# Kernel tuning notes

Measured on AMD Instinct MI355X. Metric: run time of the kernel, lower is better.

## Reference

```python
import jax, jax.numpy as jnp
import numpy as np

B, T, DK, DV, N = 4, 1024, 128, 128, 65536
TOPK = 32

def setup_inputs() -> dict:
    key = jax.random.key(0)
    k1, k2, k3 = jax.random.split(key, 3)
    q = jax.random.normal(k1, (B, T, DK), dtype=jnp.float32)
    keys = jax.random.normal(k2, (N, DK), dtype=jnp.float32)
    values = jax.random.normal(k3, (N, DV), dtype=jnp.float32)
    return {"q": q, "keys": keys, "values": values, "topk": TOPK}

def reference(q, keys, values, topk):
    # scores: [B, T, N] dense dot-product score matrix
    scores = jnp.einsum('btd,nd->btn', q, keys)
    k = min(topk, keys.shape[0])
    _, idx = jax.lax.top_k(scores, k)          # idx: [B, T, k]
    K_mem = keys[idx]                          # [B, T, k, Dk] gather
    V_mem = values[idx]                        # [B, T, k, Dv] gather
    return (K_mem, V_mem)
```

## Files before the change

### kernel.cpp

```cpp
#include <hip/hip_runtime.h>
#include <float.h>

#define NQ      4096
#define NKEYS   65536
#define DKDIM   128
#define DVDIM   128
#define TOPK_N  32
#define NSPLIT  16
#define KPS     (NKEYS / NSPLIT)
#define BQ      128
#define NCAND   (NSPLIT * TOPK_N)
#define NARROW  64
#define NOUT    ((size_t)NQ * TOPK_N * DKDIM)
#define KPT     64
#define NT      (KPS / KPT)

typedef __attribute__((ext_vector_type(8))) short short8;
typedef __attribute__((ext_vector_type(4))) float v4f;

__device__ inline unsigned short f2bf(float f) {
    unsigned int u = __float_as_uint(f);
    return (unsigned short)((u + 0x7FFFu + ((u >> 16) & 1u)) >> 16);
}

__device__ inline unsigned packpk(float s, unsigned li) {
    unsigned u = __float_as_uint(s);
    u = ((int)u < 0) ? ~u : (u | 0x80000000u);
    return (u & 0xFFFFF000u) | (4095u - li);
}
__device__ inline float unpack_lb(unsigned pk) {
    const unsigned m = pk & 0xFFFFF000u;
    const unsigned b = (m & 0x80000000u) ? (m & 0x7FFFFFFFu) : ~m;
    return __uint_as_float(b);
}

#define CEXU(p, s, desc) {                                                  \
    const unsigned _o = (unsigned)__shfl_xor((int)(p), (s));                \
    const bool _first = (p) > _o;                                           \
    const bool _keep  = (_first == (((l16 & (s)) == 0) == (desc)));         \
    (p) = _keep ? (p) : _o; }
#define CEXUI(pa, pb) { if ((pb) > (pa)) { const unsigned _t=(pa); (pa)=(pb); (pb)=_t; } }

__device__ __forceinline__ void sortmergeU(
    unsigned& p0, unsigned& p1, const int cc,
    const unsigned* __restrict__ bqr, const int l16)
{
    unsigned s0 = (l16      < cc) ? bqr[l16]      : 0u;
    unsigned s1 = (l16 + 16 < cc) ? bqr[l16 + 16] : 0u;

    CEXU(s0, 1, ((l16 & 2) == 0)); CEXU(s1, 1, ((l16 & 2) == 0));
    CEXU(s0, 2, ((l16 & 4) == 0)); CEXU(s1, 2, ((l16 & 4) == 0));
    CEXU(s0, 1, ((l16 & 4) == 0)); CEXU(s1, 1, ((l16 & 4) == 0));
    CEXU(s0, 4, ((l16 & 8) == 0)); CEXU(s1, 4, ((l16 & 8) == 0));
    CEXU(s0, 2, ((l16 & 8) == 0)); CEXU(s1, 2, ((l16 & 8) == 0));
    CEXU(s0, 1, ((l16 & 8) == 0)); CEXU(s1, 1, ((l16 & 8) == 0));
    CEXU(s0, 8, true);  CEXU(s1, 8, false);
    CEXU(s0, 4, true);  CEXU(s1, 4, false);
    CEXU(s0, 2, true);  CEXU(s1, 2, false);
    CEXU(s0, 1, true);  CEXU(s1, 1, false);
    CEXUI(s0, s1);
    CEXU(s0, 8, true);  CEXU(s1, 8, true);
    CEXU(s0, 4, true);  CEXU(s1, 4, true);
    CEXU(s0, 2, true);  CEXU(s1, 2, true);
    CEXU(s0, 1, true);  CEXU(s1, 1, true);

    unsigned c0 = (unsigned)__shfl_xor((int)s1, 15);
    unsigned c1 = (unsigned)__shfl_xor((int)s0, 15);

    CEXUI(p0, c0);
    CEXUI(p1, c1);
    CEXUI(p0, p1);
    CEXU(p0, 8, true); CEXU(p1, 8, true);
    CEXU(p0, 4, true); CEXU(p1, 4, true);
    CEXU(p0, 2, true); CEXU(p1, 2, true);
    CEXU(p0, 1, true); CEXU(p1, 1, true);
}

__global__ __launch_bounds__(256) void convert_kernel(
    const float* __restrict__ q, const float* __restrict__ keys,
    unsigned short* __restrict__ qbf, unsigned short* __restrict__ kbf)
{
    const size_t QG = (size_t)NQ * DKDIM / 8;
    const size_t KG = (size_t)NKEYS * DKDIM / 8;
    const size_t g  = (size_t)blockIdx.x * 256 + threadIdx.x;
    if (g >= QG + KG) return;
    const float* src;
    unsigned short* dst;
    if (g < QG) { src = q + g * 8;         dst = qbf + g * 8; }
    else        { const size_t h = g - QG; src = keys + h * 8; dst = kbf + h * 8; }
    const float4 a = ((const float4*)src)[0];
    const float4 b = ((const float4*)src)[1];
    short8 o;
    o[0] = (short)f2bf(a.x); o[1] = (short)f2bf(a.y);
    o[2] = (short)f2bf(a.z); o[3] = (short)f2bf(a.w);
    o[4] = (short)f2bf(b.x); o[5] = (short)f2bf(b.y);
    o[6] = (short)f2bf(b.z); o[7] = (short)f2bf(b.w);
    *(short8*)dst = o;
}

__global__ __launch_bounds__(512, 4) void score_select_kernel(
    const unsigned short* __restrict__ qbf, const unsigned short* __restrict__ kbf,
    unsigned* __restrict__ cand)
{
    __shared__ unsigned short kst[2][KPT * DKDIM];
    __shared__ unsigned bq[BQ][33];

    const int tid  = threadIdx.x;
    const int wave = tid >> 6;
    const int lane = tid & 63;
    const int l16  = lane & 15;
    const int quad = lane >> 4;

    const int lin   = blockIdx.y * gridDim.x + blockIdx.x;
    const int split = ((lin & 7) << 1) | (lin >> 8);
    const int qgrp  = (lin >> 3) & 31;
    const int q0    = qgrp * BQ + wave * 16;
    const int nbase = split * KPS;

    unsigned* __restrict__ bqr = &bq[wave * 16 + l16][0];

    short8 afrag[4];
#pragma unroll
    for (int t = 0; t < 4; ++t)
        afrag[t] = *(const short8*)(qbf + (size_t)(q0 + l16) * DKDIM + t * 32 + quad * 8);

    unsigned pk0[4], pk1[4];
#pragma unroll
    for (int r = 0; r < 4; ++r) { pk0[r] = 0u; pk1[r] = 0u; }
    float vmf = -FLT_MAX;
    int   cnt = 0;

    auto select32 = [&](const v4f a1, const v4f a2, const int n0loc) {
        const int h0 = a1[0] > vmf, h1 = a1[1] > vmf, h2 = a1[2] > vmf, h3 = a1[3] > vmf;
        const int h4 = a2[0] > vmf, h5 = a2[1] > vmf, h6 = a2[2] > vmf, h7 = a2[3] > vmf;
        const int nh = h0 + h1 + h2 + h3 + h4 + h5 + h6 + h7;
        const int s16   = __shfl_xor(nh, 16);
        const int psum  = nh + s16;
        const int sx32  = __shfl_xor(psum, 32);
        const int nhcol = psum + sx32;
        if (__ballot(cnt + nhcol > 32)) {
#pragma unroll
            for (int r = 0; r < 4; ++r) {
                const int cc = __shfl(cnt, quad * 4 + r);
                sortmergeU(pk0[r], pk1[r], cc, &bq[wave * 16 + quad * 4 + r][0], l16);
            }
            const unsigned t0 = (unsigned)__shfl((int)pk1[0], (l16 >> 2) * 16 + 15);
            const unsigned t1 = (unsigned)__shfl((int)pk1[1], (l16 >> 2) * 16 + 15);
            const unsigned t2 = (unsigned)__shfl((int)pk1[2], (l16 >> 2) * 16 + 15);
            const unsigned t3 = (unsigned)__shfl((int)pk1[3], (l16 >> 2) * 16 + 15);
            const unsigned a01 = (l16 & 1) ? t1 : t0;
            const unsigned a23 = (l16 & 1) ? t3 : t2;
            vmf = unpack_lb((l16 & 2) ? a23 : a01);
            cnt = 0;
        }
        int pos = cnt + ((quad & 1) ? s16 : 0) + ((quad & 2) ? sx32 : 0);
        const unsigned lb = (unsigned)(n0loc + quad * 4);
        if (h0) { bqr[pos] = packpk(a1[0], lb);      ++pos; }
        if (h1) { bqr[pos] = packpk(a1[1], lb + 1);  ++pos; }
        if (h2) { bqr[pos] = packpk(a1[2], lb + 2);  ++pos; }
        if (h3) { bqr[pos] = packpk(a1[3], lb + 3);  ++pos; }
        if (h4) { bqr[pos] = packpk(a2[0], lb + 16); ++pos; }
        if (h5) { bqr[pos] = packpk(a2[1], lb + 17); ++pos; }
        if (h6) { bqr[pos] = packpk(a2[2], lb + 18); ++pos; }
        if (h7) { bqr[pos] = packpk(a2[3], lb + 19); }
        cnt += nhcol;
    };

    const unsigned short* ksrc = kbf + (size_t)nbase * DKDIM;
    const int c0 = tid, c1 = tid + 512;
    const int d0 = ((c0 >> 4) * 128) + (((c0 & 15) ^ ((c0 >> 4) & 7)) * 8);
    const int d1 = ((c1 >> 4) * 128) + (((c1 & 15) ^ ((c1 >> 4) & 7)) * 8);
    const int sx = l16 & 7;

    {
        const short8 a = *(const short8*)(ksrc + c0 * 8);
        const short8 b = *(const short8*)(ksrc + c1 * 8);
        *(short8*)&kst[0][d0] = a;
        *(short8*)&kst[0][d1] = b;
    }
    __syncthreads();

    int cur = 0;
    for (int t = 0; t < NT; ++t) {
        short8 nA, nB;
        const bool more = (t + 1 < NT);
        if (more) {
            const unsigned short* s = ksrc + (size_t)(t + 1) * (KPT * DKDIM);
            nA = *(const short8*)(s + c0 * 8);
            nB = *(const short8*)(s + c1 * 8);
        }
#pragma unroll
        for (int half = 0; half < 2; ++half) {
            const unsigned short* kr0 = &kst[cur][(half * 32 + l16) * 128];
            const unsigned short* kr1 = &kst[cur][(half * 32 + 16 + l16) * 128];
            v4f acc1 = {0.f, 0.f, 0.f, 0.f};
            v4f acc2 = {0.f, 0.f, 0.f, 0.f};
#pragma unroll
            for (int tt = 0; tt < 4; ++tt) {
                const short8 b0 = *(const short8*)(kr0 + ((quad + tt * 4) ^ sx) * 8);
                const short8 b1 = *(const short8*)(kr1 + ((quad + tt * 4) ^ sx) * 8);
                acc1 = __builtin_amdgcn_mfma_f32_16x16x32_bf16(b0, afrag[tt], acc1, 0, 0, 0);
                acc2 = __builtin_amdgcn_mfma_f32_16x16x32_bf16(b1, afrag[tt], acc2, 0, 0, 0);
            }
            select32(acc1, acc2, t * KPT + half * 32);
        }
        if (more) {
            *(short8*)&kst[cur ^ 1][d0] = nA;
            *(short8*)&kst[cur ^ 1][d1] = nB;
        }
        __syncthreads();
        cur ^= 1;
    }

#pragma unroll
    for (int r = 0; r < 4; ++r) {
        const int cc = __shfl(cnt, quad * 4 + r);
        sortmergeU(pk0[r], pk1[r], cc, &bq[wave * 16 + quad * 4 + r][0], l16);
        const size_t base = ((size_t)(q0 + quad * 4 + r) * NSPLIT + split) * TOPK_N;
        cand[base + l16]      = pk0[r];
        cand[base + 16 + l16] = pk1[r];
    }
}

__global__ __launch_bounds__(512) void rescore_gather_kernel(
    const float* __restrict__ qg, const float* __restrict__ keys,
    const float* __restrict__ values, const unsigned* __restrict__ cand,
    float* __restrict__ out)
{
    __shared__ float    qrow[DKDIM];
    __shared__ unsigned spk[NCAND];
    __shared__ int      spn[NCAND];
    __shared__ int      ssi[TOPK_N];
    const int bt  = blockIdx.x;
    const int tid = threadIdx.x;

    if (tid < DKDIM) qrow[tid] = qg[(size_t)bt * DKDIM + tid];

    unsigned pk = cand[(size_t)bt * NCAND + tid];
    int      n  = (tid >> 5) * KPS + (int)(4095u - (pk & 0xFFFu));

    for (int k = 2; k <= NCAND; k <<= 1) {
        for (int j = k >> 1; j > 0; j >>= 1) {
            unsigned opk; int on;
            if (j >= 64) {
                __syncthreads();
                spk[tid] = pk; spn[tid] = n;
                __syncthreads();
                opk = spk[tid ^ j]; on = spn[tid ^ j];
            } else {
                opk = (unsigned)__shfl_xor((int)pk, j);
                on  = __shfl_xor(n, j);
            }
            const bool dir  = ((tid & k) == 0);
            const bool mineFirst = (pk > opk) || (pk == opk && n < on);
            const bool keep = (((tid & j) == 0) == (mineFirst == dir));
            if (!keep) { pk = opk; n = on; }
        }
    }
    __syncthreads();

    float sc = -FLT_MAX;
    if (tid < NARROW) {
        const float4* krow = (const float4*)(keys + (size_t)n * DKDIM);
        float s = 0.f;
#pragma unroll
        for (int d4 = 0; d4 < DKDIM / 4; ++d4) {
            const float4 k4 = krow[d4];
            const float4 q4 = *(const float4*)&qrow[4 * d4];
            s = fmaf(q4.x, k4.x, s);
            s = fmaf(q4.y, k4.y, s);
            s = fmaf(q4.z, k4.z, s);
            s = fmaf(q4.w, k4.w, s);
        }
        sc = s;
    }

    if (tid < 64) {
        for (int k = 2; k <= NARROW; k <<= 1) {
            for (int j = k >> 1; j > 0; j >>= 1) {
                const float of = __shfl_xor(sc, j);
                const int   on = __shfl_xor(n, j);
                const bool dir  = ((tid & k) == 0);
                const bool mineFirst = (sc > of) || (sc == of && n < on);
                const bool keep = (((tid & j) == 0) == (mineFirst == dir));
                if (!keep) { sc = of; n = on; }
            }
        }
        if (tid < TOPK_N) ssi[tid] = n;
    }
    __syncthreads();

    const int lane = tid & 31;
    const int rb   = tid >> 5;
#pragma unroll
    for (int r = 0; r < 2; ++r) {
        const int row = rb + 16 * r;
        const int nn  = ssi[row];
        const float4 kv = *(const float4*)(keys   + (size_t)nn * DKDIM + 4 * lane);
        const float4 vv = *(const float4*)(values + (size_t)nn * DVDIM + 4 * lane);
        const size_t ob = ((size_t)bt * TOPK_N + row) * DKDIM + 4 * lane;
        *(float4*)(out + ob)        = kv;
        *(float4*)(out + NOUT + ob) = vv;
    }
}

extern "C" void kernel_launch(void* const* d_in, const int* in_sizes, int n_in,
                              void* d_out, int out_size, void* d_ws, size_t ws_size,
                              hipStream_t stream)
{
    const float* q      = (const float*)d_in[0];
    const float* keys   = (const float*)d_in[1];
    const float* values = (const float*)d_in[2];
    float* out = (float*)d_out;

    unsigned short* qbf = (unsigned short*)d_ws;
    unsigned short* kbf = (unsigned short*)((char*)d_ws + (1u << 20));
    unsigned* cand = (unsigned*)((char*)d_ws + (17u << 20));

    const int cvt_groups = (NQ + NKEYS) * DKDIM / 8;
    convert_kernel<<<(cvt_groups + 255) / 256, 256, 0, stream>>>(q, keys, qbf, kbf);
    score_select_kernel<<<dim3(NQ / BQ, NSPLIT), 512, 0, stream>>>(qbf, kbf, cand);
    rescore_gather_kernel<<<NQ, 512, 0, stream>>>(q, keys, values, cand, out);
}
```

Measured before the change: 534.3 us.

## Sort candidates per wave in registers, removing block-level syncs in rescore

The rescore/gather kernel now gives each query to a single 64-lane wave, with four queries per 256-thread block, instead of one query per 512-thread block. The 512-candidate bitonic sort runs with each lane holding eight elements in registers. Strides of 64 and above become in-register compare-swaps, so the shared-memory exchange and __syncthreads pairs go away. The wave keeps the top 64 by approximate score, rescores them in fp32, and sorts and gathers without any block barrier. The cost is more registers per thread and more shuffle work per wave, in exchange for fewer barriers and less shared memory.

Result: no change. 542.7 us (+1.6%).

```diff
diff --git a/kernel.cpp b/kernel.cpp
--- a/kernel.cpp
+++ b/kernel.cpp
@@ -10,7 +10,6 @@
 #define KPS     (NKEYS / NSPLIT)
 #define BQ      128
 #define NCAND   (NSPLIT * TOPK_N)
-#define NARROW  64
 #define NOUT    ((size_t)NQ * TOPK_N * DKDIM)
 #define KPT     64
 #define NT      (KPS / KPT)
@@ -222,51 +221,99 @@
     }
 }
 
-__global__ __launch_bounds__(512) void rescore_gather_kernel(
+__global__ __launch_bounds__(256) void rescore_gather_kernel(
     const float* __restrict__ qg, const float* __restrict__ keys,
     const float* __restrict__ values, const unsigned* __restrict__ cand,
     float* __restrict__ out)
 {
-    __shared__ float    qrow[DKDIM];
-    __shared__ unsigned spk[NCAND];
-    __shared__ int      spn[NCAND];
-    __shared__ int      ssi[TOPK_N];
-    const int bt  = blockIdx.x;
-    const int tid = threadIdx.x;
-
-    if (tid < DKDIM) qrow[tid] = qg[(size_t)bt * DKDIM + tid];
-
-    unsigned pk = cand[(size_t)bt * NCAND + tid];
-    int      n  = (tid >> 5) * KPS + (int)(4095u - (pk & 0xFFFu));
-
-    for (int k = 2; k <= NCAND; k <<= 1) {
+    __shared__ float qsh[4][DKDIM];
+    const int tid  = threadIdx.x;
+    const int wave = tid >> 6;
+    const int lane = tid & 63;
+    const int qidx = blockIdx.x * 4 + wave;
+
+    qsh[wave][lane]      = qg[(size_t)qidx * DKDIM + lane];
+    qsh[wave][lane + 64] = qg[(size_t)qidx * DKDIM + lane + 64];
+    __syncthreads();
+
+    unsigned pk[8]; int nn[8];
+#pragma unroll
+    for (int i = 0; i < 8; ++i) {
+        const int e = i * 64 + lane;
+        const unsigned p = cand[(size_t)qidx * NCAND + e];
+        pk[i] = p;
+        nn[i] = (e >> 5) * KPS + (int)(4095u - (p & 0xFFFu));
+    }
+
+#pragma unroll
+    for (int k = 2; k <= 256; k <<= 1) {
+#pragma unroll
         for (int j = k >> 1; j > 0; j >>= 1) {
-            unsigned opk; int on;
             if (j >= 64) {
-                __syncthreads();
-                spk[tid] = pk; spn[tid] = n;
-                __syncthreads();
-                opk = spk[tid ^ j]; on = spn[tid ^ j];
+                const int m = j >> 6;
+#pragma unroll
+                for (int i = 0; i < 8; ++i) {
+                    if ((i & m) == 0) {
+                        const int i2 = i | m;
+                        const bool dir = (((i << 6) & k) == 0);
+                        const bool first = (pk[i] > pk[i2]) ||
+                                           (pk[i] == pk[i2] && nn[i] < nn[i2]);
+                        if (first != dir) {
+                            const unsigned tp = pk[i]; pk[i] = pk[i2]; pk[i2] = tp;
+                            const int      tn = nn[i]; nn[i] = nn[i2]; nn[i2] = tn;
+                        }
+                    }
+                }
             } else {
-                opk = (unsigned)__shfl_xor((int)pk, j);
-                on  = __shfl_xor(n, j);
+#pragma unroll
+                for (int i = 0; i < 8; ++i) {
+                    const unsigned opk = (unsigned)__shfl_xor((int)pk[i], j);
+                    const int      onn = __shfl_xor(nn[i], j);
+                    const bool dir   = ((((i << 6) | lane) & k) == 0);
+                    const bool upper = ((lane & j) == 0);
+                    const bool mineFirst = (pk[i] > opk) ||
+                                           (pk[i] == opk && nn[i] < onn);
+                    if (upper != (mineFirst == dir)) { pk[i] = opk; nn[i] = onn; }
+                }
             }
-            const bool dir  = ((tid & k) == 0);
-            const bool mineFirst = (pk > opk) || (pk == opk && n < on);
-            const bool keep = (((tid & j) == 0) == (mineFirst == dir));
-            if (!keep) { pk = opk; n = on; }
-        }
-    }
-    __syncthreads();
-
-    float sc = -FLT_MAX;
-    if (tid < NARROW) {
+        }
+    }
+#pragma unroll
+    for (int i = 0; i < 4; ++i) {
+        const int i2 = i + 4;
+        const bool first = (pk[i] > pk[i2]) || (pk[i] == pk[i2] && nn[i] < nn[i2]);
+        if (!first) {
+            const unsigned tp = pk[i]; pk[i] = pk[i2]; pk[i2] = tp;
+            const int      tn = nn[i]; nn[i] = nn[i2]; nn[i2] = tn;
+        }
+    }
+#pragma unroll
+    for (int i = 0; i < 2; ++i) {
+        const int i2 = i + 2;
+        const bool first = (pk[i] > pk[i2]) || (pk[i] == pk[i2] && nn[i] < nn[i2]);
+        if (!first) {
+            const unsigned tp = pk[i]; pk[i] = pk[i2]; pk[i2] = tp;
+            const int      tn = nn[i]; nn[i] = nn[i2]; nn[i2] = tn;
+        }
+    }
+    {
+        const bool first = (pk[0] > pk[1]) || (pk[0] == pk[1] && nn[0] < nn[1]);
+        if (!first) {
+            const unsigned tp = pk[0]; pk[0] = pk[1]; pk[1] = tp;
+            const int      tn = nn[0]; nn[0] = nn[1]; nn[1] = tn;
+        }
+    }
+
+    int   n = nn[0];
+    float sc;
+    {
         const float4* krow = (const float4*)(keys + (size_t)n * DKDIM);
+        const float4* qr   = (const float4*)&qsh[wave][0];
         float s = 0.f;
 #pragma unroll
         for (int d4 = 0; d4 < DKDIM / 4; ++d4) {
             const float4 k4 = krow[d4];
-            const float4 q4 = *(const float4*)&qrow[4 * d4];
+            const float4 q4 = qr[d4];
             s = fmaf(q4.x, k4.x, s);
             s = fmaf(q4.y, k4.y, s);
             s = fmaf(q4.z, k4.z, s);
@@ -275,30 +322,28 @@
         sc = s;
     }
 
-    if (tid < 64) {
-        for (int k = 2; k <= NARROW; k <<= 1) {
-            for (int j = k >> 1; j > 0; j >>= 1) {
-                const float of = __shfl_xor(sc, j);
-                const int   on = __shfl_xor(n, j);
-                const bool dir  = ((tid & k) == 0);
-                const bool mineFirst = (sc > of) || (sc == of && n < on);
-                const bool keep = (((tid & j) == 0) == (mineFirst == dir));
-                if (!keep) { sc = of; n = on; }
-            }
-        }
-        if (tid < TOPK_N) ssi[tid] = n;
-    }
-    __syncthreads();
-
-    const int lane = tid & 31;
-    const int rb   = tid >> 5;
-#pragma unroll
-    for (int r = 0; r < 2; ++r) {
-        const int row = rb + 16 * r;
-        const int nn  = ssi[row];
-        const float4 kv = *(const float4*)(keys   + (size_t)nn * DKDIM + 4 * lane);
-        const float4 vv = *(const float4*)(values + (size_t)nn * DVDIM + 4 * lane);
-        const size_t ob = ((size_t)bt * TOPK_N + row) * DKDIM + 4 * lane;
+#pragma unroll
+    for (int k = 2; k <= 64; k <<= 1) {
+#pragma unroll
+        for (int j = k >> 1; j > 0; j >>= 1) {
+            const float of = __shfl_xor(sc, j);
+            const int   on = __shfl_xor(n, j);
+            const bool dir   = ((lane & k) == 0);
+            const bool upper = ((lane & j) == 0);
+            const bool mineFirst = (sc > of) || (sc == of && n < on);
+            if (upper != (mineFirst == dir)) { sc = of; n = on; }
+        }
+    }
+
+    const int l32  = lane & 31;
+    const int half = lane >> 5;
+#pragma unroll
+    for (int t = 0; t < 16; ++t) {
+        const int row = 2 * t + half;
+        const int nr  = __shfl(n, row);
+        const float4 kv = *(const float4*)(keys   + (size_t)nr * DKDIM + 4 * l32);
+        const float4 vv = *(const float4*)(values + (size_t)nr * DVDIM + 4 * l32);
+        const size_t ob = ((size_t)qidx * TOPK_N + row) * DKDIM + 4 * l32;
         *(float4*)(out + ob)        = kv;
         *(float4*)(out + NOUT + ob) = vv;
     }
@@ -320,5 +365,5 @@
     const int cvt_groups = (NQ + NKEYS) * DKDIM / 8;
     convert_kernel<<<(cvt_groups + 255) / 256, 256, 0, stream>>>(q, keys, qbf, kbf);
     score_select_kernel<<<dim3(NQ / BQ, NSPLIT), 512, 0, stream>>>(qbf, kbf, cand);
-    rescore_gather_kernel<<<NQ, 512, 0, stream>>>(q, keys, values, cand, out);
-}
+    rescore_gather_kernel<<<NQ / 4, 256, 0, stream>>>(q, keys, values, cand, out);
+}
```
